# Performance work log

Measured on AMD Instinct MI355X. Metric: run time of the kernel, lower is better.

The kernel has to match this reference:

```python
import jax, jax.numpy as jnp
import numpy as np

B, E, S, W, M, C, O = 2048, 16, 512, 512, 64, 64, 8

def hardsigmoid(x):
    return jnp.clip((x + 3.0) / 6.0, 0.0, 1.0)

def swish(x):
    return x * jax.nn.sigmoid(x)

def setup_inputs() -> dict:
    key = jax.random.key(0)
    ks = jax.random.split(key, 16)
    scale = 1.0  # 1/(in_channels*out_channels) with in=out=1
    d = {}
    d["x"] = jax.random.normal(ks[0], (B, E * S), jnp.float32)
    d["codes"] = jax.random.normal(ks[1], (E, C), jnp.float32) * 0.1
    d["p_w"] = jax.random.normal(ks[2], (2 * W, 2 * S), jnp.float32) * 0.02
    d["p_b"] = jnp.zeros((2 * W,), jnp.float32)
    d["com0"] = jax.random.uniform(ks[3], (M, 2), jnp.float32) * scale
    d["code0"] = jax.random.uniform(ks[4], (C, M, 2), jnp.float32) * scale
    d["filt0"] = -3.0 * jnp.ones((M,), jnp.float32)
    d["com1"] = jax.random.uniform(ks[5], (M, 2), jnp.float32) * scale
    d["code1"] = jax.random.uniform(ks[6], (C, M, 2), jnp.float32) * scale
    d["filt1"] = -3.0 * jnp.ones((M,), jnp.float32)
    d["w0_w"] = jax.random.normal(ks[7], (2 * W, 2 * W), jnp.float32) * 0.02
    d["w0_b"] = jnp.zeros((2 * W,), jnp.float32)
    d["w1_w"] = jax.random.normal(ks[8], (2 * W, 2 * W), jnp.float32) * 0.02
    d["w1_b"] = jnp.zeros((2 * W,), jnp.float32)
    # fc1: Conv1d(2W -> (O//2)*W, k=1, groups=W): per group 2 in -> O//2 out
    d["fc1_w"] = jax.random.normal(ks[9], (W, O // 2, 2), jnp.float32) * 0.1
    d["fc1_b"] = jnp.zeros((W * (O // 2),), jnp.float32)
    d["fc2_w"] = jax.random.normal(ks[10], (O, W * (O // 2)), jnp.float32) * 0.02
    d["fc2_b"] = jnp.zeros((O,), jnp.float32)
    return d

def spectral(x3, codes, com, codew, filt):
    # x3: [B, E, L] with in_channels=out_channels=1; L = 2*W
    L = x3.shape[-1]
    m = filt.shape[0]
    xf = jnp.fft.rfft(x3, axis=-1)                      # [B, E, L//2+1] complex64
    lam = hardsigmoid(filt)                              # [m]
    com_c = com[:, 0] + 1j * com[:, 1]                   # [m]
    env = jnp.einsum('ec,cmk->emk', codes, codew)        # [E, m, 2]
    env_c = env[..., 0] + 1j * env[..., 1]               # [E, m]
    xm = xf[:, :, :m]                                    # [B, E, m]
    out_m = lam * xm * com_c + (1.0 - lam) * xm * env_c[None]
    out_f = jnp.zeros_like(xf).at[:, :, :m].set(out_m)
    return jnp.fft.irfft(out_f, n=L, axis=-1)            # [B, E, L]

def reference(x, codes, p_w, p_b, com0, code0, filt0, com1, code1, filt1,
              w0_w, w0_b, w1_w, w1_b, fc1_w, fc1_b, fc2_w, fc2_b):
    bsz = x.shape[0]
    e = codes.shape[0]
    s = x.shape[1] // e
    xv = x.reshape(bsz, e, s)
    grid = jnp.broadcast_to(jnp.linspace(0.0, 1.0, s, dtype=x.dtype), (bsz, e, s))
    h = jnp.concatenate([xv, grid], axis=-1).reshape(bsz * e, 2 * s)
    h = h @ p_w.T + p_b                                  # [BE, 2W]
    twoW = h.shape[-1]
    h3 = h.reshape(bsz, e, twoW)
    x1 = spectral(h3, codes, com0, code0, filt0)
    x2 = h @ w0_w.T + w0_b
    h3 = swish(x1 + x2.reshape(bsz, e, twoW))
    h = h3.reshape(bsz * e, twoW)
    x1 = spectral(h3, codes, com1, code1, filt1)
    x2 = h @ w1_w.T + w1_b
    h = (x1 + x2.reshape(bsz, e, twoW)).reshape(bsz * e, twoW)
    # grouped pointwise fc1: groups = W, 2 in-ch per group -> O//2 out-ch per group
    wd = fc1_w.shape[0]
    hg = h.reshape(bsz * e, wd, 2)
    h = jnp.einsum('ngk,gok->ngo', hg, fc1_w).reshape(bsz * e, -1) + fc1_b
    h = swish(h)
    h = h @ fc2_w.T + fc2_b                              # [BE, O]
    return h.reshape(bsz, -1)                            # [B, E*O]
```

## Files before the change

### kernel.cpp

```cpp
#include <hip/hip_runtime.h>
#include <hip/hip_bf16.h>
#include <cstdint>


typedef __bf16 bf16;
typedef __attribute__((ext_vector_type(8))) __bf16 bf16x8;
typedef __attribute__((ext_vector_type(4))) __bf16 bf16x4;
typedef __attribute__((ext_vector_type(4))) float f32x4;

#define N_ROWS 32768

__device__ __forceinline__ void gl_lds16(const void* g, void* l) {
    __builtin_amdgcn_global_load_lds(
        (const __attribute__((address_space(1))) void*)g,
        (__attribute__((address_space(3))) void*)l,
        16, 0, 0);
}

__device__ __forceinline__ float swishf(float v) {
    return v / (1.f + __expf(-v));
}


__global__ __launch_bounds__(256) void build_cmix(const float* __restrict__ codes,
                                                  const float* __restrict__ com,
                                                  const float* __restrict__ code,
                                                  const float* __restrict__ filt,
                                                  float2* __restrict__ cmix) {
    int t = blockIdx.x * 256 + threadIdx.x;
    if (t >= 16 * 64) return;
    int e = t >> 6, m = t & 63;
    float er = 0.f, ei = 0.f;
    for (int c = 0; c < 64; ++c) {
        float cd = codes[e * 64 + c];
        er += cd * code[(c * 64 + m) * 2 + 0];
        ei += cd * code[(c * 64 + m) * 2 + 1];
    }
    float f = filt[m];
    float lam = fminf(fmaxf((f + 3.f) * (1.f / 6.f), 0.f), 1.f);
    float cr = lam * com[m * 2 + 0] + (1.f - lam) * er;
    float ci = lam * com[m * 2 + 1] + (1.f - lam) * ei;
    float g = (m == 0) ? (1.f / 1024.f) : (2.f / 1024.f);
    cmix[t] = make_float2(g * cr, g * ci);
}

__global__ __launch_bounds__(256) void build_fb2(float* __restrict__ Fb32,
                                                 bf16* __restrict__ Fbb) {
    int t = blockIdx.x * 256 + threadIdx.x;
    int rr = t >> 10, s = t & 1023;
    int k = rr >> 1;
    int ph = (k * s) & 1023;
    float ang = (float)ph * 6.1359231515425649e-3f;
    float v = (rr & 1) ? -sinf(ang) : cosf(ang);
    Fb32[t] = v;
    Fbb[t] = (bf16)v;
}

__global__ __launch_bounds__(256) void build_bcat(const float* __restrict__ w,
                                                  bf16* __restrict__ out) {
    int t = blockIdx.x * 256 + threadIdx.x;
    if (t >= 1024 * 1152) return;
    int j = t / 1152, c = t % 1152;
    float v;
    if (c < 1024) {
        v = w[j * 1024 + c];
    } else {
        int cc = c - 1024, k = cc >> 1;
        int ph = (k * j) & 1023;
        float ang = (float)ph * 6.1359231515425649e-3f;
        v = (cc & 1) ? -sinf(ang) : cosf(ang);
    }
    out[t] = (bf16)v;
}

__global__ __launch_bounds__(256) void build_g(const float* __restrict__ Fb32,
                                               const float* __restrict__ p_w,
                                               float* __restrict__ G32) {
    int c = blockIdx.x * 256 + threadIdx.x;
    int k2 = blockIdx.y;
    const float* fb = Fb32 + k2 * 1024;
    float a = 0.f;
    #pragma unroll 8
    for (int w = 0; w < 1024; ++w)
        a += fb[w] * p_w[(size_t)w * 1024 + c];
    G32[k2 * 512 + c] = a;
}

__global__ __launch_bounds__(256) void build_bias1a(const float* __restrict__ p_w,
                                                    const float* __restrict__ p_b,
                                                    float* __restrict__ bias1) {
    int w = (blockIdx.x * 256 + threadIdx.x) >> 6;
    int lane = threadIdx.x & 63;
    const float* src = p_w + (size_t)w * 1024 + 512 + lane * 8;
    float4 v0 = *(const float4*)(src);
    float4 v1 = *(const float4*)(src + 4);
    float s0 = (float)(lane * 8) * (1.f / 511.f);
    const float st = 1.f / 511.f;
    float a = v0.x * s0 + v0.y * (s0 + st) + v0.z * (s0 + 2 * st) + v0.w * (s0 + 3 * st)
            + v1.x * (s0 + 4 * st) + v1.y * (s0 + 5 * st) + v1.z * (s0 + 6 * st) + v1.w * (s0 + 7 * st);
    #pragma unroll
    for (int msk = 1; msk < 64; msk <<= 1) a += __shfl_xor(a, msk);
    if (lane == 0) bias1[w] = p_b[w] + a;
}

__global__ __launch_bounds__(256) void build_bias1b(const float* __restrict__ Fb32,
                                                    float* __restrict__ bias1) {
    int k2 = blockIdx.x * 4 + (threadIdx.x >> 6);
    int lane = threadIdx.x & 63;
    const float* fb = Fb32 + (size_t)k2 * 1024 + lane * 16;
    const float* bb = bias1 + lane * 16;
    float a = 0.f;
    #pragma unroll
    for (int j = 0; j < 4; ++j) {
        float4 f = *(const float4*)(fb + 4 * j);
        float4 b = *(const float4*)(bb + 4 * j);
        a += f.x * b.x + f.y * b.y + f.z * b.z + f.w * b.w;
    }
    #pragma unroll
    for (int msk = 1; msk < 64; msk <<= 1) a += __shfl_xor(a, msk);
    if (lane == 0) {
        bias1[1024 + k2] = a;
        bias1[1152 + k2] = 0.f;
    }
}

__global__ __launch_bounds__(256) void build_wp(const float* __restrict__ p_w,
                                                const float* __restrict__ G32,
                                                bf16* __restrict__ WP) {
    int t = blockIdx.x * 256 + threadIdx.x;
    if (t >= 1280 * 512) return;
    int r = t >> 9, c = t & 511;
    float v = (r < 1024) ? p_w[(size_t)r * 1024 + c]
            : (r < 1152) ? G32[(r - 1024) * 512 + c] : 0.f;
    WP[t] = (bf16)v;
}

__global__ __launch_bounds__(256) void convert_x(const float* __restrict__ x,
                                                 bf16* __restrict__ A0) {
    int t = blockIdx.x * 256 + threadIdx.x;
    const float4* xp = (const float4*)(x + (size_t)t * 8);
    float4 a = xp[0], b = xp[1];
    bf16x8 o;
    o[0] = (bf16)a.x; o[1] = (bf16)a.y; o[2] = (bf16)a.z; o[3] = (bf16)a.w;
    o[4] = (bf16)b.x; o[5] = (bf16)b.y; o[6] = (bf16)b.z; o[7] = (bf16)b.w;
    *(bf16x8*)(A0 + (size_t)t * 8) = o;
}

template<int ACT, int HASMIX>
__global__ __launch_bounds__(512, 2)
void gemm256(const bf16* __restrict__ A, int lda,
             const bf16* __restrict__ Bt, int ldb,
             const float* __restrict__ bias,
             bf16* __restrict__ Cout, int ldc,
             const float2* __restrict__ cmix, int ncols,
             int K, int NX, int NY) {
    __shared__ bf16 sA[4][256 * 32];
    __shared__ bf16 sB[4][256 * 32];
    const int tid = threadIdx.x;
    const int wave = tid >> 6, lane = tid & 63;
    const int wm = wave >> 2, wn = wave & 3;

    int tx, ty;
    if ((NX & 7) == 0) {
        int xcd = blockIdx.x & 7;
        int pos = blockIdx.x >> 3;
        ty = pos % NY;
        tx = (pos / NY) * 8 + xcd;
    } else {
        tx = blockIdx.x % NX;
        ty = blockIdx.x / NX;
    }
    const int rowA0 = tx * 256;
    const int rowB0 = ty * 256;

    f32x4 acc[8][4];
    #pragma unroll
    for (int m = 0; m < 8; ++m)
        #pragma unroll
        for (int n = 0; n < 4; ++n)
            acc[m][n] = f32x4{0.f, 0.f, 0.f, 0.f};

    const int srq = lane >> 2;
    const int ssl = (lane & 3) ^ (srq & 3);
    const bf16* gA = A + (size_t)(rowA0 + wave * 16 + srq) * lda + ssl * 8;
    const bf16* gB = Bt + (size_t)(rowB0 + wave * 16 + srq) * ldb + ssl * 8;

    const int NT = K / 32;
    auto STAGE = [&](int t) {
        const int slot = t & 3;
        const size_t ko = (size_t)t * 32;
        gl_lds16(gA + ko,                       &sA[slot][(wave * 16) * 32]);
        gl_lds16(gA + (size_t)128 * lda + ko,   &sA[slot][(128 + wave * 16) * 32]);
        gl_lds16(gB + ko,                       &sB[slot][(wave * 16) * 32]);
        gl_lds16(gB + (size_t)128 * ldb + ko,   &sB[slot][(128 + wave * 16) * 32]);
    };

    STAGE(0);
    STAGE(1);

    const int p = lane & 15, q = lane >> 4;
    const int axr = (p & 3) << 4;

    for (int t = 0; t < NT; ++t) {
        if (t + 2 < NT) STAGE(t + 2);
        if (t < NT - 2)       { asm volatile("s_waitcnt vmcnt(8)" ::: "memory"); }
        else if (t == NT - 2) { asm volatile("s_waitcnt vmcnt(4)" ::: "memory"); }
        else                  { asm volatile("s_waitcnt vmcnt(0)" ::: "memory"); }
        __builtin_amdgcn_s_barrier();
        __builtin_amdgcn_sched_barrier(0);
        const char* sa = (const char*)sA[t & 3];
        const char* sb = (const char*)sB[t & 3];
        bf16x8 af[8], bfr[4];
        #pragma unroll
        for (int m = 0; m < 8; ++m) {
            int off = (((wm * 128 + m * 16 + p) * 32 + q * 8) * 2) ^ axr;
            af[m] = *(const bf16x8*)(sa + off);
        }
        #pragma unroll
        for (int n = 0; n < 4; ++n) {
            int off = (((wn * 64 + n * 16 + p) * 32 + q * 8) * 2) ^ axr;
            bfr[n] = *(const bf16x8*)(sb + off);
        }
        asm volatile("s_waitcnt lgkmcnt(0)" ::: "memory");
        __builtin_amdgcn_sched_barrier(0);
        __builtin_amdgcn_s_setprio(1);
        #pragma unroll
        for (int m = 0; m < 8; ++m)
            #pragma unroll
            for (int n = 0; n < 4; ++n)
                acc[m][n] = __builtin_amdgcn_mfma_f32_16x16x32_bf16(af[m], bfr[n], acc[m][n], 0, 0, 0);
        __builtin_amdgcn_s_setprio(0);
        __builtin_amdgcn_sched_barrier(0);
    }

    const int rowb = rowA0 + wm * 128;
    const int colb = rowB0 + wn * 64;
    #pragma unroll
    for (int m = 0; m < 8; ++m) {
        #pragma unroll
        for (int n = 0; n < 4; ++n) {
            int col = colb + n * 16 + p;
            float bv = bias ? bias[col] : 0.f;
            #pragma unroll
            for (int r = 0; r < 4; ++r) {
                int row = rowb + m * 16 + q * 4 + r;
                float v = acc[m][n][r] + bv;
                if (HASMIX) {
                    float pp = __shfl_xor(v, 1);
                    if (col >= 1024) {
                        int k = (col - 1024) >> 1;
                        float2 c = cmix[(row & 15) * 64 + k];
                        v = v * c.x + (((p & 1) == 0) ? -pp * c.y : pp * c.y);
                    }
                    if (col < ncols) Cout[(size_t)row * ldc + col] = (bf16)v;
                } else {
                    if (ACT) v = swishf(v);
                    Cout[(size_t)row * ldc + col] = (bf16)v;
                }
            }
        }
    }
}

__global__ __launch_bounds__(256)
void gemm_mix(const bf16* __restrict__ A, int lda,
              const bf16* __restrict__ Bt, int ldb,
              void* __restrict__ Cout, int ldc,
              const float2* __restrict__ cmix,
              int K) {
    __shared__ bf16 sA[128 * 64];
    __shared__ bf16 sB[128 * 64];
    const int tid = threadIdx.x;
    const int wave = tid >> 6;
    const int lane = tid & 63;
    const int wm = wave >> 1, wn = wave & 1;
    const int rowA0 = blockIdx.x * 128;

    f32x4 acc[4][4];
    #pragma unroll
    for (int m = 0; m < 4; ++m)
        #pragma unroll
        for (int n = 0; n < 4; ++n)
            acc[m][n] = f32x4{0.f, 0.f, 0.f, 0.f};

    const int srow = wave * 32 + (lane >> 3);
    const int scol = (lane & 7) * 8;
    const bf16* gA = A + (size_t)(rowA0 + srow) * lda + scol;
    const bf16* gB = Bt + (size_t)srow * ldb + scol;
    bf16* lA = &sA[(wave * 32) * 64];
    bf16* lB = &sB[(wave * 32) * 64];

    for (int k0 = 0; k0 < K; k0 += 64) {
        __syncthreads();
        #pragma unroll
        for (int i = 0; i < 4; ++i) {
            gl_lds16(gA + (size_t)i * 8 * lda + k0, lA + i * 8 * 64);
            gl_lds16(gB + (size_t)i * 8 * ldb + k0, lB + i * 8 * 64);
        }
        __syncthreads();
        #pragma unroll
        for (int kk = 0; kk < 64; kk += 32) {
            bf16x8 af[4], bfr[4];
            #pragma unroll
            for (int m = 0; m < 4; ++m)
                af[m] = *(const bf16x8*)&sA[(wm * 64 + m * 16 + (lane & 15)) * 64 + kk + ((lane >> 4) * 8)];
            #pragma unroll
            for (int n = 0; n < 4; ++n)
                bfr[n] = *(const bf16x8*)&sB[(wn * 64 + n * 16 + (lane & 15)) * 64 + kk + ((lane >> 4) * 8)];
            #pragma unroll
            for (int m = 0; m < 4; ++m)
                #pragma unroll
                for (int n = 0; n < 4; ++n)
                    acc[m][n] = __builtin_amdgcn_mfma_f32_16x16x32_bf16(af[m], bfr[n], acc[m][n], 0, 0, 0);
        }
    }

    const int rowb = rowA0 + wm * 64;
    #pragma unroll
    for (int m = 0; m < 4; ++m) {
        #pragma unroll
        for (int n = 0; n < 4; ++n) {
            int col = wn * 64 + n * 16 + (lane & 15);
            int k = col >> 1;
            #pragma unroll
            for (int r = 0; r < 4; ++r) {
                float v = acc[m][n][r];
                float pp = __shfl_xor(v, 1);
                int row = rowb + m * 16 + (lane >> 4) * 4 + r;
                float2 c = cmix[(row & 15) * 64 + k];
                float val = v * c.x + (((lane & 1) == 0) ? -pp * c.y : pp * c.y);
                ((bf16*)Cout)[(size_t)row * ldc + col] = (bf16)val;
            }
        }
    }
}

__global__ __launch_bounds__(256) void fc_fused(const bf16* __restrict__ H,
                                                const float* __restrict__ w1,
                                                const float* __restrict__ b1,
                                                const float* __restrict__ w2,
                                                const float* __restrict__ b2,
                                                float* __restrict__ out) {
    __shared__ bf16 sw2[8][2048];
    __shared__ bf16 ss[2048];
    int tid = threadIdx.x;
    for (int i = tid * 4; i < 8 * 2048; i += 1024) {
        float4 v = *(const float4*)(w2 + i);
        bf16x4 b = {(bf16)v.x, (bf16)v.y, (bf16)v.z, (bf16)v.w};
        *(bf16x4*)&sw2[0][i] = b;
    }

    float wv[16];
    const float4* w1p = (const float4*)(w1 + tid * 16);
    *(float4*)&wv[0]  = w1p[0];
    *(float4*)&wv[4]  = w1p[1];
    *(float4*)&wv[8]  = w1p[2];
    *(float4*)&wv[12] = w1p[3];
    float bb[8];
    const float4* b1p = (const float4*)(b1 + tid * 8);
    *(float4*)&bb[0] = b1p[0];
    *(float4*)&bb[4] = b1p[1];
    __syncthreads();

    for (int r = 0; r < 16; ++r) {
        int n = blockIdx.x * 16 + r;
        bf16x4 hv = *(const bf16x4*)(H + (size_t)n * 1024 + tid * 4);
        float hh[4] = {(float)hv[0], (float)hv[1], (float)hv[2], (float)hv[3]};
        bf16x8 sb;
        #pragma unroll
        for (int jj = 0; jj < 8; ++jj) {
            float h0 = hh[(jj >> 2) * 2];
            float h1 = hh[(jj >> 2) * 2 + 1];
            float t = h0 * wv[2 * jj] + h1 * wv[2 * jj + 1] + bb[jj];
            sb[jj] = (bf16)swishf(t);
        }
        *(bf16x8*)&ss[tid * 8] = sb;
        __syncthreads();
        int o8 = tid >> 5, l5 = tid & 31;
        float p = 0.f;
        #pragma unroll
        for (int i = 0; i < 16; ++i) {
            bf16x4 a = *(const bf16x4*)&ss[4 * l5 + 128 * i];
            bf16x4 b = *(const bf16x4*)&sw2[o8][4 * l5 + 128 * i];
            p += (float)a[0] * (float)b[0] + (float)a[1] * (float)b[1]
               + (float)a[2] * (float)b[2] + (float)a[3] * (float)b[3];
        }
        #pragma unroll
        for (int msk = 1; msk < 32; msk <<= 1) p += __shfl_xor(p, msk);
        if (l5 == 0) out[(size_t)n * 8 + o8] = p + b2[o8];
        __syncthreads();
    }
}


extern "C" void kernel_launch(void* const* d_in, const int* in_sizes, int n_in,
                              void* d_out, int out_size, void* d_ws, size_t ws_size,
                              hipStream_t stream) {
    const float* x     = (const float*)d_in[0];
    const float* codes = (const float*)d_in[1];
    const float* p_w   = (const float*)d_in[2];
    const float* p_b   = (const float*)d_in[3];
    const float* com0  = (const float*)d_in[4];
    const float* code0 = (const float*)d_in[5];
    const float* filt0 = (const float*)d_in[6];
    const float* com1  = (const float*)d_in[7];
    const float* code1 = (const float*)d_in[8];
    const float* filt1 = (const float*)d_in[9];
    const float* w0_w  = (const float*)d_in[10];
    const float* w0_b  = (const float*)d_in[11];
    const float* w1_w  = (const float*)d_in[12];
    const float* w1_b  = (const float*)d_in[13];
    const float* fc1w  = (const float*)d_in[14];
    const float* fc1b  = (const float*)d_in[15];
    const float* fc2w  = (const float*)d_in[16];
    const float* fc2b  = (const float*)d_in[17];
    float* out = (float*)d_out;

    char* ws = (char*)d_ws;
    bf16*  WP   = (bf16*)(ws + 0);
    bf16*  B0   = (bf16*)(ws + 1310720);
    bf16*  B1   = (bf16*)(ws + 3670016);
    bf16*  Fbb  = (bf16*)(ws + 6029312);
    float* Fb32 = (float*)(ws + 6291456);
    float* G32  = (float*)(ws + 6815744);
    float* bias1= (float*)(ws + 7077888);
    float2* cm0 = (float2*)(ws + 7083008);
    float2* cm1 = (float2*)(ws + 7091200);
    const size_t CB = 7099392;

    const size_t PER_ROW = 2048 + 2304 + 2304;
    long rmax = 0;
    if (ws_size > CB) rmax = (long)((ws_size - CB) / PER_ROW) / 256 * 256;
    if (rmax > N_ROWS) rmax = N_ROWS;
    if (rmax < 256) {
        hipMemsetAsync(d_out, 0, (size_t)out_size * sizeof(float), stream);
        return;
    }
    const int R = (int)rmax;

    build_cmix<<<4, 256, 0, stream>>>(codes, com0, code0, filt0, cm0);
    build_cmix<<<4, 256, 0, stream>>>(codes, com1, code1, filt1, cm1);
    build_fb2<<<512, 256, 0, stream>>>(Fb32, Fbb);
    build_bcat<<<4608, 256, 0, stream>>>(w0_w, B0);
    build_bcat<<<4608, 256, 0, stream>>>(w1_w, B1);
    build_g<<<dim3(2, 128), 256, 0, stream>>>(Fb32, p_w, G32);
    build_bias1a<<<256, 256, 0, stream>>>(p_w, p_b, bias1);
    build_bias1b<<<32, 256, 0, stream>>>(Fb32, bias1);
    build_wp<<<2560, 256, 0, stream>>>(p_w, G32, WP);

    char* cb = ws + CB;
    for (int row0 = 0; row0 < N_ROWS; row0 += R) {
        const int r = (N_ROWS - row0 < R) ? (N_ROWS - row0) : R;
        bf16*  A0  = (bf16*)cb;
        bf16*  H3b = (bf16*)cb;
        bf16*  A1  = (bf16*)(cb + (size_t)R * 2048);
        bf16*  A2  = (bf16*)(cb + (size_t)R * 2048 + (size_t)R * 2304);
        const int NX = r / 256;

        convert_x<<<r / 4, 256, 0, stream>>>(x + (size_t)row0 * 512, A0);

        gemm256<0, 1><<<NX * 5, 512, 0, stream>>>(
            A0, 512, WP, 512, bias1, A1, 1152, cm0, 1152, 512, NX, 5);
        gemm256<1, 0><<<NX * 4, 512, 0, stream>>>(
            A1, 1152, B0, 1152, w0_b, A2, 1152, nullptr, 1024, 1152, NX, 4);
        gemm_mix<<<dim3(r / 128, 1), 256, 0, stream>>>(
            A2, 1152, Fbb, 1024, (void*)(A2 + 1024), 1152, cm1, 1024);
        gemm256<0, 0><<<NX * 4, 512, 0, stream>>>(
            A2, 1152, B1, 1152, w1_b, H3b, 1024, nullptr, 1024, 1152, NX, 4);
        fc_fused<<<r / 16, 256, 0, stream>>>(H3b, fc1w, fc1b, fc2w, fc2b, out + (size_t)row0 * 8);
    }
}
```

Baseline: 509.5 us.

## Software-pipeline LDS fragment loads with MFMA and change LDS swizzle pattern

Restructures the GEMM main loop so each K-tile's MFMAs are split into two halves. The A rows 4-7 fragments load while the first half computes, and the next tile's B and A rows 0-3 fragments are prefetched into double-buffered registers during the second half. The aim is to hide LDS read latency behind matrix instructions instead of waiting on lgkmcnt(0) before every tile. It also changes the XOR swizzle to use bits 1-2 of the row index, which should reduce LDS bank conflicts. In exchange, register pressure rises from the extra fragment buffers, and the loop assumes NT is even.

```diff
diff --git a/kernel.cpp b/kernel.cpp
--- a/kernel.cpp
+++ b/kernel.cpp
@@ -181,7 +181,7 @@
             acc[m][n] = f32x4{0.f, 0.f, 0.f, 0.f};
 
     const int srq = lane >> 2;
-    const int ssl = (lane & 3) ^ (srq & 3);
+    const int ssl = (lane & 3) ^ ((lane >> 3) & 3);
     const bf16* gA = A + (size_t)(rowA0 + wave * 16 + srq) * lda + ssl * 8;
     const bf16* gB = Bt + (size_t)(rowB0 + wave * 16 + srq) * ldb + ssl * 8;
 
@@ -189,49 +189,82 @@
     auto STAGE = [&](int t) {
         const int slot = t & 3;
         const size_t ko = (size_t)t * 32;
-        gl_lds16(gA + ko,                       &sA[slot][(wave * 16) * 32]);
-        gl_lds16(gA + (size_t)128 * lda + ko,   &sA[slot][(128 + wave * 16) * 32]);
-        gl_lds16(gB + ko,                       &sB[slot][(wave * 16) * 32]);
-        gl_lds16(gB + (size_t)128 * ldb + ko,   &sB[slot][(128 + wave * 16) * 32]);
+        gl_lds16(gA + ko,                     &sA[slot][(wave * 16) * 32]);
+        gl_lds16(gA + (size_t)128 * lda + ko, &sA[slot][(128 + wave * 16) * 32]);
+        gl_lds16(gB + ko,                     &sB[slot][(wave * 16) * 32]);
+        gl_lds16(gB + (size_t)128 * ldb + ko, &sB[slot][(128 + wave * 16) * 32]);
     };
+
+    const int p = lane & 15, q = lane >> 4;
+    const int axr = ((p >> 1) & 3) << 4;
+
+    bf16x8 a03x[4], bfx[4], a03y[4], bfy[4], a47[4];
 
     STAGE(0);
     STAGE(1);
-
-    const int p = lane & 15, q = lane >> 4;
-    const int axr = (p & 3) << 4;
-
-    for (int t = 0; t < NT; ++t) {
-        if (t + 2 < NT) STAGE(t + 2);
-        if (t < NT - 2)       { asm volatile("s_waitcnt vmcnt(8)" ::: "memory"); }
-        else if (t == NT - 2) { asm volatile("s_waitcnt vmcnt(4)" ::: "memory"); }
-        else                  { asm volatile("s_waitcnt vmcnt(0)" ::: "memory"); }
-        __builtin_amdgcn_s_barrier();
-        __builtin_amdgcn_sched_barrier(0);
-        const char* sa = (const char*)sA[t & 3];
-        const char* sb = (const char*)sB[t & 3];
-        bf16x8 af[8], bfr[4];
-        #pragma unroll
-        for (int m = 0; m < 8; ++m) {
-            int off = (((wm * 128 + m * 16 + p) * 32 + q * 8) * 2) ^ axr;
-            af[m] = *(const bf16x8*)(sa + off);
-        }
-        #pragma unroll
-        for (int n = 0; n < 4; ++n) {
-            int off = (((wn * 64 + n * 16 + p) * 32 + q * 8) * 2) ^ axr;
-            bfr[n] = *(const bf16x8*)(sb + off);
-        }
-        asm volatile("s_waitcnt lgkmcnt(0)" ::: "memory");
-        __builtin_amdgcn_sched_barrier(0);
-        __builtin_amdgcn_s_setprio(1);
-        #pragma unroll
-        for (int m = 0; m < 8; ++m)
-            #pragma unroll
-            for (int n = 0; n < 4; ++n)
-                acc[m][n] = __builtin_amdgcn_mfma_f32_16x16x32_bf16(af[m], bfr[n], acc[m][n], 0, 0, 0);
-        __builtin_amdgcn_s_setprio(0);
-        __builtin_amdgcn_sched_barrier(0);
-    }
+    asm volatile("s_waitcnt vmcnt(4)" ::: "memory");
+    __builtin_amdgcn_s_barrier();
+    __builtin_amdgcn_sched_barrier(0);
+    {
+        const char* sa = (const char*)sA[0];
+        const char* sb = (const char*)sB[0];
+        #pragma unroll
+        for (int n = 0; n < 4; ++n)
+            bfx[n] = *(const bf16x8*)(sb + ((((wn * 64 + n * 16 + p) * 32 + q * 8) * 2) ^ axr));
+        #pragma unroll
+        for (int m = 0; m < 4; ++m)
+            a03x[m] = *(const bf16x8*)(sa + ((((wm * 128 + m * 16 + p) * 32 + q * 8) * 2) ^ axr));
+    }
+    __builtin_amdgcn_sched_barrier(0);
+
+    #define TILE_BODY(T, CF_A03, CF_B, NF_A03, NF_B)                                   \
+    {                                                                                  \
+        if ((T) + 2 < NT) STAGE((T) + 2);                                              \
+        if ((T) + 2 < NT) { asm volatile("s_waitcnt vmcnt(4)" ::: "memory"); }         \
+        else              { asm volatile("s_waitcnt vmcnt(0)" ::: "memory"); }         \
+        __builtin_amdgcn_s_barrier();                                                  \
+        __builtin_amdgcn_sched_barrier(0);                                             \
+        const char* sa_ = (const char*)sA[(T) & 3];                                    \
+        _Pragma("unroll")                                                              \
+        for (int m = 0; m < 4; ++m)                                                    \
+            a47[m] = *(const bf16x8*)(sa_ + ((((wm * 128 + (m + 4) * 16 + p) * 32 + q * 8) * 2) ^ axr)); \
+        asm volatile("s_waitcnt lgkmcnt(4)" ::: "memory");                             \
+        __builtin_amdgcn_sched_barrier(0);                                             \
+        __builtin_amdgcn_s_setprio(1);                                                 \
+        _Pragma("unroll")                                                              \
+        for (int m = 0; m < 4; ++m)                                                    \
+            _Pragma("unroll")                                                          \
+            for (int n = 0; n < 4; ++n)                                                \
+                acc[m][n] = __builtin_amdgcn_mfma_f32_16x16x32_bf16(CF_A03[m], CF_B[n], acc[m][n], 0, 0, 0); \
+        __builtin_amdgcn_s_setprio(0);                                                 \
+        asm volatile("s_waitcnt lgkmcnt(0)" ::: "memory");                             \
+        __builtin_amdgcn_sched_barrier(0);                                             \
+        if ((T) + 1 < NT) {                                                            \
+            const char* sa1 = (const char*)sA[((T) + 1) & 3];                          \
+            const char* sb1 = (const char*)sB[((T) + 1) & 3];                          \
+            _Pragma("unroll")                                                          \
+            for (int n = 0; n < 4; ++n)                                                \
+                NF_B[n] = *(const bf16x8*)(sb1 + ((((wn * 64 + n * 16 + p) * 32 + q * 8) * 2) ^ axr)); \
+            _Pragma("unroll")                                                          \
+            for (int m = 0; m < 4; ++m)                                                \
+                NF_A03[m] = *(const bf16x8*)(sa1 + ((((wm * 128 + m * 16 + p) * 32 + q * 8) * 2) ^ axr)); \
+        }                                                                              \
+        __builtin_amdgcn_sched_barrier(0);                                             \
+        __builtin_amdgcn_s_setprio(1);                                                 \
+        _Pragma("unroll")                                                              \
+        for (int m = 0; m < 4; ++m)                                                    \
+            _Pragma("unroll")                                                          \
+            for (int n = 0; n < 4; ++n)                                                \
+                acc[m + 4][n] = __builtin_amdgcn_mfma_f32_16x16x32_bf16(a47[m], CF_B[n], acc[m + 4][n], 0, 0, 0); \
+        __builtin_amdgcn_s_setprio(0);                                                 \
+        __builtin_amdgcn_sched_barrier(0);                                             \
+    }
+
+    for (int tt = 0; tt < NT; tt += 2) {
+        TILE_BODY(tt,     a03x, bfx, a03y, bfy)
+        TILE_BODY(tt + 1, a03y, bfy, a03x, bfx)
+    }
+    #undef TILE_BODY
 
     const int rowb = rowA0 + wm * 128;
     const int colb = rowB0 + wn * 64;
```

New measurement: 509.0 us. Within noise of the previous version (-0.1%).
